# Kernel tuning notes

Hardware: AMD Instinct MI355X
Metric: run time of the kernel (lower is better)

The kernel has to match this reference:

```python
import math
import jax, jax.numpy as jnp
import numpy as np

BLOCK_K = 128  # key/value block size; S_k % BLOCK_K == 0 so no padding/mask needed


def setup_inputs() -> dict:
    key = jax.random.key(0)
    kq, kk, kv = jax.random.split(key, 3)
    B, S, H, Hkv, D = 1, 4096, 16, 8, 128
    return {
        "query": jax.random.normal(kq, (B, S, H, D), dtype=jnp.float32),
        "key": jax.random.normal(kk, (B, S, Hkv, D), dtype=jnp.float32),
        "value": jax.random.normal(kv, (B, S, Hkv, D), dtype=jnp.float32),
    }


def _ring_attention(query, key, value, block_k=BLOCK_K):
    # query: [B, Sq, H, D]; key/value: [B, Sk, Hkv, D]
    scale = 1.0 / math.sqrt(query.shape[-1])
    reps = query.shape[2] // key.shape[2]
    if reps > 1:  # GQA: repeat kv heads to match query heads
        key = jnp.repeat(key, reps, axis=2)
        value = jnp.repeat(value, reps, axis=2)
    q = jnp.transpose(query, (0, 2, 1, 3))   # [B, H, Sq, D]
    k = jnp.transpose(key, (0, 2, 1, 3))     # [B, H, Sk, D]
    v = jnp.transpose(value, (0, 2, 1, 3))
    B, H, Sq, D = q.shape
    Sk = k.shape[2]
    nk = Sk // block_k
    # split keys/values into blocks, block axis leading for scan
    kb = k.reshape(B, H, nk, block_k, D).transpose(2, 0, 1, 3, 4)
    vb = v.reshape(B, H, nk, block_k, D).transpose(2, 0, 1, 3, 4)
    m0 = jnp.full((B, H, Sq), -jnp.inf, dtype=jnp.float32)
    l0 = jnp.zeros((B, H, Sq), dtype=jnp.float32)
    o0 = jnp.zeros((B, H, Sq, D), dtype=jnp.float32)

    def step(carry, kv_blk):
        m, l, o = carry
        k_blk, v_blk = kv_blk
        scores = jnp.einsum('bhqd,bhkd->bhqk', q, k_blk) * scale
        m_new = jnp.maximum(m, jnp.max(scores, axis=-1))
        alpha = jnp.exp(m - m_new)                     # rescale factor (0 on first step)
        p = jnp.exp(scores - m_new[..., None])
        l = l * alpha + jnp.sum(p, axis=-1)
        o = o * alpha[..., None] + jnp.einsum('bhqk,bhkd->bhqd', p, v_blk)
        return (m_new, l, o), None

    (m, l, o), _ = jax.lax.scan(step, (m0, l0, o0), (kb, vb))
    out = o / l[..., None]
    return jnp.transpose(out, (0, 2, 1, 3))  # [B, Sq, H, D]


def reference(query, key, value):
    return _ring_attention(query, key, value)
```

## Files before the change

kernel.cpp:

```cpp
#include <hip/hip_runtime.h>
#include <math.h>


namespace {
constexpr int NH  = 16;
constexpr int NKV = 8;
constexpr int DH  = 128;
constexpr int SK  = 4096;
constexpr int TQ  = 128;
constexpr int NT  = 256;

constexpr int BKM   = 32;
constexpr int NKTM  = SK / BKM;
constexpr int TILEM = BKM * DH;
constexpr size_t WS_NEED = (size_t)2 * NKV * NKTM * TILEM * sizeof(_Float16);

constexpr int NIT   = NKTM / 2;
constexpr int CHUNK = 2 * TILEM;

constexpr int BK  = 64;
constexpr int NKT = SK / BK;

typedef _Float16 half8 __attribute__((ext_vector_type(8)));
typedef _Float16 half4 __attribute__((ext_vector_type(4)));
typedef _Float16 half2v __attribute__((ext_vector_type(2)));
typedef __fp16   fp16x2 __attribute__((ext_vector_type(2)));
typedef float  floatx4 __attribute__((ext_vector_type(4)));
typedef unsigned short ushort8 __attribute__((ext_vector_type(8)));

#define MFMA16(a, b, c) __builtin_amdgcn_mfma_f32_16x16x32_f16((a), (b), (c), 0, 0, 0)

#define BARRIER_LGKM() asm volatile("s_waitcnt lgkmcnt(0)\n\ts_barrier" ::: "memory")

__global__ __launch_bounds__(256)
void prepack_kv(const float* __restrict__ Kg, const float* __restrict__ Vg,
                _Float16* __restrict__ Kx, _Float16* __restrict__ Vx) {
  __shared__ __align__(16) _Float16 Kb[BKM * 128];
  __shared__ __align__(16) _Float16 Vb[BKM * 132];
  const int id = blockIdx.x;
  const int hk = id & 7;
  const int kt = id >> 3;
  const int t  = threadIdx.x;

#pragma unroll
  for (int it = 0; it < 4; ++it) {
    const int r  = it * 8 + (t >> 5);
    const int c4 = t & 31;
    const size_t src = (((size_t)(kt * BKM + r) * NKV + hk) * DH) + c4 * 4;
    const float4 kf = *reinterpret_cast<const float4*>(Kg + src);
    const float4 vf = *reinterpret_cast<const float4*>(Vg + src);
    half4 kh;
    kh[0] = (_Float16)kf.x; kh[1] = (_Float16)kf.y;
    kh[2] = (_Float16)kf.z; kh[3] = (_Float16)kf.w;
    *reinterpret_cast<half4*>(&Kb[r * 128 + c4 * 4]) = kh;
    half2v v0, v1;
    v0[0] = (_Float16)vf.x; v0[1] = (_Float16)vf.y;
    v1[0] = (_Float16)vf.z; v1[1] = (_Float16)vf.w;
    *reinterpret_cast<half2v*>(&Vb[r * 132 + c4 * 4])     = v0;
    *reinterpret_cast<half2v*>(&Vb[r * 132 + c4 * 4 + 2]) = v1;
  }
  __syncthreads();

  {
    _Float16* out = Kx + (size_t)(hk * NKTM + kt) * TILEM;
#pragma unroll
    for (int it = 0; it < 2; ++it) {
      const int L  = it * 2048 + t * 8;
      const int r  = L >> 7;
      const int gp = (L >> 3) & 15;
      const int c8 = gp ^ (r & 7);
      *reinterpret_cast<half8*>(out + L) =
          *reinterpret_cast<const half8*>(&Kb[r * 128 + c8 * 8]);
    }
  }
  {
    _Float16* out = Vx + (size_t)(hk * NKTM + kt) * TILEM;
    const int dp = t >> 2;
    const int g  = t & 3;
    const int ql = g ^ (dp & 3);
    const int d  = dp * 2;
    ushort8 lo, hi;
#pragma unroll
    for (int j = 0; j < 8; ++j) {
      const int key = ((j >> 2) * 16) + ql * 4 + (j & 3);
      const unsigned v = *reinterpret_cast<const unsigned*>(&Vb[key * 132 + d]);
      lo[j] = (unsigned short)(v & 0xffffu);
      hi[j] = (unsigned short)(v >> 16);
    }
    *reinterpret_cast<ushort8*>(out + d * 32 + g * 8)       = lo;
    *reinterpret_cast<ushort8*>(out + (d + 1) * 32 + g * 8) = hi;
  }
}

__global__ __launch_bounds__(NT, 2)
void flash_fwd_pk(const float* __restrict__ Qg,
                  const _Float16* __restrict__ Kx,
                  const _Float16* __restrict__ Vx,
                  float* __restrict__ Og) {
  __shared__ __align__(16) _Float16 KsB[2][CHUNK];
  __shared__ __align__(16) _Float16 VtB[2][CHUNK];

  const int tid  = threadIdx.x;
  const int wave = tid >> 6;
  const int lane = tid & 63;
  const int m16  = lane & 15;
  const int quad = lane >> 4;
  const int hsw  = m16 & 7;
  const int sw2  = (m16 >> 1) & 3;

  const int id = blockIdx.x;
  const int hk = id & 7;
  const int h  = (hk << 1) | ((id >> 3) & 1);
  const int qt = id >> 4;
  const int qr0 = qt * TQ + wave * 32;

  const float4* Q4 = reinterpret_cast<const float4*>(Qg);
  const float scale2 = (float)(0.08838834764831845 * 1.4426950408889634);

  half8 qa[2][4];
#pragma unroll
  for (int mt = 0; mt < 2; ++mt) {
#pragma unroll
    for (int kc = 0; kc < 4; ++kc) {
      const int r = qr0 + mt * 16 + m16;
      const int b = (r * NH + h) * (DH / 4) + kc * 8 + quad * 2;
      float4 x = Q4[b], y = Q4[b + 1];
      half8 f;
      f[0] = (_Float16)(x.x * scale2); f[1] = (_Float16)(x.y * scale2);
      f[2] = (_Float16)(x.z * scale2); f[3] = (_Float16)(x.w * scale2);
      f[4] = (_Float16)(y.x * scale2); f[5] = (_Float16)(y.y * scale2);
      f[6] = (_Float16)(y.z * scale2); f[7] = (_Float16)(y.w * scale2);
      qa[mt][kc] = f;
    }
  }

  floatx4 o[2][8];
#pragma unroll
  for (int mt = 0; mt < 2; ++mt)
#pragma unroll
    for (int nt = 0; nt < 8; ++nt) o[mt][nt] = (floatx4){0.f, 0.f, 0.f, 0.f};
  float lsum[2] = {0.f, 0.f};

  const _Float16* gK = Kx + (size_t)hk * NKTM * TILEM;
  const _Float16* gV = Vx + (size_t)hk * NKTM * TILEM;
  const int soff = tid * 8;

  half8 kr[4], vr[4];
#pragma unroll
  for (int i = 0; i < 4; ++i) {
    kr[i] = *reinterpret_cast<const half8*>(gK + i * 2048 + soff);
    vr[i] = *reinterpret_cast<const half8*>(gV + i * 2048 + soff);
  }

  for (int kt = 0; kt < NIT; ++kt) {
    const int b = kt & 1;
#pragma unroll
    for (int i = 0; i < 4; ++i) {
      *reinterpret_cast<half8*>(&KsB[b][i * 2048 + soff]) = kr[i];
      *reinterpret_cast<half8*>(&VtB[b][i * 2048 + soff]) = vr[i];
    }
    {
      const int ktn = (kt + 1 < NIT) ? kt + 1 : kt;
      const _Float16* gKt = gK + (size_t)ktn * CHUNK;
      const _Float16* gVt = gV + (size_t)ktn * CHUNK;
#pragma unroll
      for (int i = 0; i < 4; ++i) {
        kr[i] = *reinterpret_cast<const half8*>(gKt + i * 2048 + soff);
        vr[i] = *reinterpret_cast<const half8*>(gVt + i * 2048 + soff);
      }
    }
    BARRIER_LGKM();

#pragma unroll
    for (int c = 0; c < 2; ++c) {
      const _Float16* Ks = &KsB[b][c * TILEM];
      const _Float16* Vt = &VtB[b][c * TILEM];

      floatx4 s[2][2];
#pragma unroll
      for (int mt = 0; mt < 2; ++mt)
#pragma unroll
        for (int nt = 0; nt < 2; ++nt) s[mt][nt] = (floatx4){0.f, 0.f, 0.f, 0.f};
      __builtin_amdgcn_s_setprio(1);
#pragma unroll
      for (int nt = 0; nt < 2; ++nt) {
#pragma unroll
        for (int kc = 0; kc < 4; ++kc) {
          const int g = (kc * 4 + quad) ^ hsw;
          half8 kb = *reinterpret_cast<const half8*>(
              &Ks[(nt * 16 + m16) * 128 + g * 8]);
          s[0][nt] = MFMA16(kb, qa[0][kc], s[0][nt]);
          s[1][nt] = MFMA16(kb, qa[1][kc], s[1][nt]);
        }
      }
      __builtin_amdgcn_s_setprio(0);

      union H8 { half8 h; fp16x2 w[4]; };
      half8 pa[2];
#pragma unroll
      for (int mt = 0; mt < 2; ++mt) {
        float p[8];
#pragma unroll
        for (int nt = 0; nt < 2; ++nt)
#pragma unroll
          for (int r = 0; r < 4; ++r)
            p[nt * 4 + r] = __builtin_amdgcn_exp2f(s[mt][nt][r]);
        lsum[mt] += ((p[0] + p[1]) + (p[2] + p[3])) +
                    ((p[4] + p[5]) + (p[6] + p[7]));
        H8 u;
        u.w[0] = __builtin_amdgcn_cvt_pkrtz(p[0], p[1]);
        u.w[1] = __builtin_amdgcn_cvt_pkrtz(p[2], p[3]);
        u.w[2] = __builtin_amdgcn_cvt_pkrtz(p[4], p[5]);
        u.w[3] = __builtin_amdgcn_cvt_pkrtz(p[6], p[7]);
        pa[mt] = u.h;
      }

      const int gq = quad ^ sw2;
      __builtin_amdgcn_s_setprio(1);
#pragma unroll
      for (int nt = 0; nt < 8; ++nt) {
        half8 vb = *reinterpret_cast<const half8*>(
            &Vt[(nt * 16 + m16) * 32 + gq * 8]);
        o[0][nt] = MFMA16(pa[0], vb, o[0][nt]);
        o[1][nt] = MFMA16(pa[1], vb, o[1][nt]);
      }
      __builtin_amdgcn_s_setprio(0);
    }
  }

#pragma unroll
  for (int mt = 0; mt < 2; ++mt) {
    float ls = lsum[mt];
    ls += __shfl_xor(ls, 16);
    ls += __shfl_xor(ls, 32);
#pragma unroll
    for (int r = 0; r < 4; ++r) {
      const int rq = quad * 4 + r;
      const float inv = 1.f / __shfl(ls, rq);
      const int row = qr0 + mt * 16 + rq;
      const int ob = (row * NH + h) * DH + m16;
#pragma unroll
      for (int nt = 0; nt < 8; ++nt)
        Og[ob + nt * 16] = o[mt][nt][r] * inv;
    }
  }
}

constexpr int KP = 136, VP = 72, PP = 72;

__global__ __launch_bounds__(NT, 2)
void flash_fwd_fb(const float* __restrict__ Qg, const float* __restrict__ Kg,
                  const float* __restrict__ Vg, float* __restrict__ Og) {
  __shared__ _Float16 Ks[BK * KP];
  __shared__ _Float16 Vt[DH * VP];
  __shared__ _Float16 Ps[4 * 32 * PP];

  const int tid  = threadIdx.x;
  const int wave = tid >> 6;
  const int lane = tid & 63;
  const int m16  = lane & 15;
  const int quad = lane >> 4;

  const int id = blockIdx.x;
  const int hk = id & 7;
  const int h  = (hk << 1) | ((id >> 3) & 1);
  const int qt = id >> 4;
  const int qr0 = qt * TQ + wave * 32;

  const float4* Q4 = reinterpret_cast<const float4*>(Qg);
  const float4* K4 = reinterpret_cast<const float4*>(Kg);
  const float scale2 = (float)(0.08838834764831845 * 1.4426950408889634);

  half8 qa[2][4];
#pragma unroll
  for (int mt = 0; mt < 2; ++mt) {
#pragma unroll
    for (int kc = 0; kc < 4; ++kc) {
      const int r = qr0 + mt * 16 + m16;
      const int b = (r * NH + h) * (DH / 4) + kc * 8 + quad * 2;
      float4 x = Q4[b], y = Q4[b + 1];
      half8 f;
      f[0] = (_Float16)(x.x * scale2); f[1] = (_Float16)(x.y * scale2);
      f[2] = (_Float16)(x.z * scale2); f[3] = (_Float16)(x.w * scale2);
      f[4] = (_Float16)(y.x * scale2); f[5] = (_Float16)(y.y * scale2);
      f[6] = (_Float16)(y.z * scale2); f[7] = (_Float16)(y.w * scale2);
      qa[mt][kc] = f;
    }
  }

  floatx4 o[2][8];
#pragma unroll
  for (int mt = 0; mt < 2; ++mt)
#pragma unroll
    for (int nt = 0; nt < 8; ++nt) o[mt][nt] = (floatx4){0.f, 0.f, 0.f, 0.f};
  float lrow[2][4];
#pragma unroll
  for (int mt = 0; mt < 2; ++mt)
#pragma unroll
    for (int r = 0; r < 4; ++r) lrow[mt][r] = 0.f;

  const int kkey = tid >> 2, kdq = tid & 3;
  const int vdim = tid & 127, vkg = tid >> 7;

  float4 kpre[8];
  float  vpre[32];
  {
    const int kb = (kkey * NKV + hk) * (DH / 4);
#pragma unroll
    for (int j = 0; j < 8; ++j) kpre[j] = K4[kb + j * 4 + kdq];
    const int vb = (vkg * 32) * NKV * DH + hk * DH + vdim;
#pragma unroll
    for (int e = 0; e < 32; ++e) vpre[e] = Vg[vb + e * (NKV * DH)];
  }

  for (int kt = 0; kt < NKT; ++kt) {
    __syncthreads();
#pragma unroll
    for (int j = 0; j < 8; ++j) {
      fp16x2 a = __builtin_amdgcn_cvt_pkrtz(kpre[j].x, kpre[j].y);
      fp16x2 b = __builtin_amdgcn_cvt_pkrtz(kpre[j].z, kpre[j].w);
      half4 hv;
      hv[0] = (_Float16)a[0]; hv[1] = (_Float16)a[1];
      hv[2] = (_Float16)b[0]; hv[3] = (_Float16)b[1];
      *reinterpret_cast<half4*>(&Ks[kkey * KP + (j * 4 + kdq) * 4]) = hv;
    }
#pragma unroll
    for (int jj = 0; jj < 4; ++jj) {
      half8 hv;
#pragma unroll
      for (int e = 0; e < 4; ++e) {
        fp16x2 p = __builtin_amdgcn_cvt_pkrtz(vpre[jj * 8 + 2 * e],
                                              vpre[jj * 8 + 2 * e + 1]);
        hv[2 * e] = (_Float16)p[0]; hv[2 * e + 1] = (_Float16)p[1];
      }
      *reinterpret_cast<half8*>(&Vt[vdim * VP + vkg * 32 + jj * 8]) = hv;
    }
    __syncthreads();

    floatx4 s[2][4];
#pragma unroll
    for (int mt = 0; mt < 2; ++mt)
#pragma unroll
      for (int nt = 0; nt < 4; ++nt) s[mt][nt] = (floatx4){0.f, 0.f, 0.f, 0.f};
#pragma unroll
    for (int nt = 0; nt < 4; ++nt) {
#pragma unroll
      for (int kc = 0; kc < 4; ++kc) {
        half8 kb = *reinterpret_cast<const half8*>(
            &Ks[(nt * 16 + m16) * KP + kc * 32 + quad * 8]);
        s[0][nt] = MFMA16(qa[0][kc], kb, s[0][nt]);
        s[1][nt] = MFMA16(qa[1][kc], kb, s[1][nt]);
      }
    }

    {
      const int ktn = (kt + 1 < NKT) ? kt + 1 : kt;
      const int kb = ((ktn * BK + kkey) * NKV + hk) * (DH / 4);
#pragma unroll
      for (int j = 0; j < 8; ++j) kpre[j] = K4[kb + j * 4 + kdq];
      const int vb = (ktn * BK + vkg * 32) * NKV * DH + hk * DH + vdim;
#pragma unroll
      for (int e = 0; e < 32; ++e) vpre[e] = Vg[vb + e * (NKV * DH)];
    }

#pragma unroll
    for (int mt = 0; mt < 2; ++mt) {
#pragma unroll
      for (int nt = 0; nt < 4; ++nt) {
#pragma unroll
        for (int r = 0; r < 4; ++r) {
          const float p = exp2f(s[mt][nt][r]);
          s[mt][nt][r] = p;
          lrow[mt][r] += p;
        }
      }
#pragma unroll
      for (int r = 0; r < 4; ++r) {
        const int prow = (wave * 32 + mt * 16 + quad * 4 + r) * PP;
#pragma unroll
        for (int nt = 0; nt < 4; ++nt)
          Ps[prow + nt * 16 + m16] = (_Float16)s[mt][nt][r];
      }
    }

    half8 pa[2][2];
#pragma unroll
    for (int mt = 0; mt < 2; ++mt)
#pragma unroll
      for (int kc = 0; kc < 2; ++kc)
        pa[mt][kc] = *reinterpret_cast<const half8*>(
            &Ps[(wave * 32 + mt * 16 + m16) * PP + kc * 32 + quad * 8]);
#pragma unroll
    for (int nt = 0; nt < 8; ++nt) {
#pragma unroll
      for (int kc = 0; kc < 2; ++kc) {
        half8 vb = *reinterpret_cast<const half8*>(
            &Vt[(nt * 16 + m16) * VP + kc * 32 + quad * 8]);
        o[0][nt] = MFMA16(pa[0][kc], vb, o[0][nt]);
        o[1][nt] = MFMA16(pa[1][kc], vb, o[1][nt]);
      }
    }
  }

#pragma unroll
  for (int mt = 0; mt < 2; ++mt) {
#pragma unroll
    for (int r = 0; r < 4; ++r) {
      float ls = lrow[mt][r];
      ls += __shfl_xor(ls, 1);
      ls += __shfl_xor(ls, 2);
      ls += __shfl_xor(ls, 4);
      ls += __shfl_xor(ls, 8);
      const float inv = 1.f / ls;
      const int row = qr0 + mt * 16 + quad * 4 + r;
      const int ob = (row * NH + h) * DH + m16;
#pragma unroll
      for (int nt = 0; nt < 8; ++nt)
        Og[ob + nt * 16] = o[mt][nt][r] * inv;
    }
  }
}
}

extern "C" void kernel_launch(void* const* d_in, const int* in_sizes, int n_in,
                              void* d_out, int out_size, void* d_ws, size_t ws_size,
                              hipStream_t stream) {
  const float* Q = (const float*)d_in[0];
  const float* K = (const float*)d_in[1];
  const float* V = (const float*)d_in[2];
  float* O = (float*)d_out;
  if (ws_size >= WS_NEED) {
    _Float16* Kx = (_Float16*)d_ws;
    _Float16* Vx = Kx + (size_t)NKV * NKTM * TILEM;
    prepack_kv<<<1024, 256, 0, stream>>>(K, V, Kx, Vx);
    flash_fwd_pk<<<512, NT, 0, stream>>>(Q, Kx, Vx, O);
  } else {
    flash_fwd_fb<<<512, NT, 0, stream>>>(Q, K, V, O);
  }
}
```

Measured before the change: 228.7 us.

## Stream K/V tiles directly into LDS with global_load_lds double buffering

Replaces the register-staged K/V prefetch (global load into registers, then an LDS store) with direct global-to-LDS loads into the alternate buffer. The loop now waits on vmcnt plus a barrier before issuing the next tile's loads. This is meant to cut VGPR pressure and the LDS write instructions. In exchange, the wait at the top of each iteration puts global latency back on the critical path unless the loads overlap with compute. The double-buffer write into b^1 also relies on the barrier to keep it from racing with reads of the previous iteration's buffer.

Result: no change. 229.9 us (+0.5%).

```diff
diff --git a/kernel.cpp b/kernel.cpp
--- a/kernel.cpp
+++ b/kernel.cpp
@@ -28,9 +28,12 @@
 typedef float  floatx4 __attribute__((ext_vector_type(4)));
 typedef unsigned short ushort8 __attribute__((ext_vector_type(8)));
 
+typedef __attribute__((address_space(1))) unsigned gu32;
+typedef __attribute__((address_space(3))) unsigned lu32;
+
 #define MFMA16(a, b, c) __builtin_amdgcn_mfma_f32_16x16x32_f16((a), (b), (c), 0, 0, 0)
 
-#define BARRIER_LGKM() asm volatile("s_waitcnt lgkmcnt(0)\n\ts_barrier" ::: "memory")
+#define WAITDMA_BARRIER() asm volatile("s_waitcnt vmcnt(0)\n\ts_barrier" ::: "memory")
 
 __global__ __launch_bounds__(256)
 void prepack_kv(const float* __restrict__ Kg, const float* __restrict__ Vg,
@@ -101,8 +104,8 @@
   __shared__ __align__(16) _Float16 VtB[2][CHUNK];
 
   const int tid  = threadIdx.x;
+  const int lane = tid & 63;
   const int wave = tid >> 6;
-  const int lane = tid & 63;
   const int m16  = lane & 15;
   const int quad = lane >> 4;
   const int hsw  = m16 & 7;
@@ -145,31 +148,32 @@
   const _Float16* gV = Vx + (size_t)hk * NKTM * TILEM;
   const int soff = tid * 8;
 
-  half8 kr[4], vr[4];
 #pragma unroll
   for (int i = 0; i < 4; ++i) {
-    kr[i] = *reinterpret_cast<const half8*>(gK + i * 2048 + soff);
-    vr[i] = *reinterpret_cast<const half8*>(gV + i * 2048 + soff);
+    __builtin_amdgcn_global_load_lds(
+        (const gu32*)(const void*)(gK + i * 2048 + soff),
+        (lu32*)(void*)(&KsB[0][i * 2048 + soff]), 16, 0, 0);
+    __builtin_amdgcn_global_load_lds(
+        (const gu32*)(const void*)(gV + i * 2048 + soff),
+        (lu32*)(void*)(&VtB[0][i * 2048 + soff]), 16, 0, 0);
   }
 
   for (int kt = 0; kt < NIT; ++kt) {
     const int b = kt & 1;
-#pragma unroll
-    for (int i = 0; i < 4; ++i) {
-      *reinterpret_cast<half8*>(&KsB[b][i * 2048 + soff]) = kr[i];
-      *reinterpret_cast<half8*>(&VtB[b][i * 2048 + soff]) = vr[i];
-    }
-    {
-      const int ktn = (kt + 1 < NIT) ? kt + 1 : kt;
-      const _Float16* gKt = gK + (size_t)ktn * CHUNK;
-      const _Float16* gVt = gV + (size_t)ktn * CHUNK;
+    WAITDMA_BARRIER();
+    if (kt + 1 < NIT) {
+      const _Float16* gKt = gK + (size_t)(kt + 1) * CHUNK;
+      const _Float16* gVt = gV + (size_t)(kt + 1) * CHUNK;
 #pragma unroll
       for (int i = 0; i < 4; ++i) {
-        kr[i] = *reinterpret_cast<const half8*>(gKt + i * 2048 + soff);
-        vr[i] = *reinterpret_cast<const half8*>(gVt + i * 2048 + soff);
-      }
-    }
-    BARRIER_LGKM();
+        __builtin_amdgcn_global_load_lds(
+            (const gu32*)(const void*)(gKt + i * 2048 + soff),
+            (lu32*)(void*)(&KsB[b ^ 1][i * 2048 + soff]), 16, 0, 0);
+        __builtin_amdgcn_global_load_lds(
+            (const gu32*)(const void*)(gVt + i * 2048 + soff),
+            (lu32*)(void*)(&VtB[b ^ 1][i * 2048 + soff]), 16, 0, 0);
+      }
+    }
 
 #pragma unroll
     for (int c = 0; c < 2; ++c) {
```
